# Kernel tuning notes

Measured on AMD Instinct MI355X. Metric: run time of the kernel, lower is better.

Reference implementation:

```python
import jax, jax.numpy as jnp
import numpy as np

N_NODES = 50000
N_PAIRS = 625000
F = 128

def setup_inputs() -> dict:
    key = jax.random.key(0)
    k1, k2, k3, k4, k5 = jax.random.split(key, 5)
    x = jax.random.normal(k1, (N_NODES, F), dtype=jnp.float32)
    alpha_ij = jax.random.normal(k2, (N_PAIRS,), dtype=jnp.float32)
    idx_i = jax.random.randint(k3, (N_PAIRS,), 0, N_NODES, dtype=jnp.int32)
    idx_j = jax.random.randint(k4, (N_PAIRS,), 0, N_NODES, dtype=jnp.int32)
    # Dense(F, use_bias=False) kernel, shape (F_in, F_out)
    W = jax.random.normal(k5, (F, F), dtype=jnp.float32) / np.sqrt(F)
    return {"x": x, "alpha_ij": alpha_ij, "idx_i": idx_i, "idx_j": idx_j, "W": W}

def reference(x, alpha_ij, idx_i, idx_j, W):
    # dense projection on nodes (n,F) @ (F,F) -> (n,F)
    v = jnp.matmul(x, W)
    # gather neighbor values, scale by attention coeff: (n_pairs, F)
    msg = alpha_ij[:, None] * v[idx_j]
    # scatter-sum back to center atoms
    return jax.ops.segment_sum(msg, segment_ids=idx_i, num_segments=x.shape[0])
```

## Files before the change

kernel.cpp:

```cpp
#include <hip/hip_runtime.h>
#include <stdint.h>

#define FDIM 128
#define BR 64
#define SLOTS 48
#define NB_C 196
#define QC 4096
#define PPB 2048
#define P2SPLIT 4

typedef short  s8v   __attribute__((ext_vector_type(8)));
typedef float  f4v   __attribute__((ext_vector_type(4)));
typedef unsigned short u8v __attribute__((ext_vector_type(8)));

__device__ __forceinline__ unsigned short f2bf(float f) {
    union { float f; uint32_t u; } c; c.f = f;
    uint32_t u = c.u;
    return (unsigned short)((u + 0x7fffu + ((u >> 16) & 1u)) >> 16);
}
__device__ __forceinline__ float bflo2f(uint32_t g) {
    union { uint32_t u; float f; } c; c.u = g << 16; return c.f;
}
__device__ __forceinline__ float bfhi2f(uint32_t g) {
    union { uint32_t u; float f; } c; c.u = g & 0xffff0000u; return c.f;
}

__global__ __launch_bounds__(256) void prep(const float* __restrict__ W,
                                            unsigned short* __restrict__ Wt,
                                            int* __restrict__ cnt,
                                            int* __restrict__ gcur,
                                            int n_nodes) {
    int i = blockIdx.x * 256 + threadIdx.x;
    if (i < FDIM * FDIM) {
        int n = i & 127, k = i >> 7;
        Wt[n * FDIM + k] = f2bf(W[k * FDIM + n]);
    }
    if (i < n_nodes) cnt[i] = 0;
    if (i < NB_C)    gcur[i] = 0;
}

__global__ __launch_bounds__(256) void fused_gemm_pass1(
        const float* __restrict__ x,
        const unsigned short* __restrict__ Wt,
        unsigned short* __restrict__ v,
        const int* __restrict__ idx_i,
        const int* __restrict__ idx_j,
        const float* __restrict__ alpha,
        int* __restrict__ gcur,
        unsigned long long* __restrict__ qrec,
        int n_rows, int n_pairs, int GB) {
    __shared__ unsigned short As[BR][FDIM + 8];

    if ((int)blockIdx.x >= GB) {
        __shared__ int hist[NB_C];
        __shared__ int base_s[NB_C];
        const int t = threadIdx.x;
        const int start = (blockIdx.x - GB) * PPB;

        if (t < NB_C) hist[t] = 0;
        __syncthreads();

        unsigned long long rec[8];
        int bkt[8];
#pragma unroll
        for (int i = 0; i < 8; ++i) {
            int p = start + t + i * 256;
            bkt[i] = -1;
            if (p < n_pairs) {
                int ii = idx_i[p];
                int b  = ii >> 8;
                bkt[i] = b;
                rec[i] = (unsigned long long)(uint32_t)(idx_j[p] | ((ii & 255) << 16) | (b << 24))
                       | ((unsigned long long)(uint32_t)__float_as_int(alpha[p]) << 32);
                atomicAdd(&hist[b], 1);
            }
        }
        __syncthreads();
        if (t < NB_C) {
            int h = hist[t];
            base_s[t] = (h > 0) ? atomicAdd(&gcur[t], h) : 0;
            hist[t] = 0;
        }
        __syncthreads();
#pragma unroll
        for (int i = 0; i < 8; ++i) {
            int b = bkt[i];
            if (b >= 0) {
                int lp  = atomicAdd(&hist[b], 1);
                int pos = base_s[b] + lp;
                if (pos < QC)
                    qrec[(size_t)b * QC + pos] = rec[i];
            }
        }
        return;
    }

    const int t = threadIdx.x;
    const int row0 = blockIdx.x * BR;
    {
        int r  = t >> 2;
        int c0 = (t & 3) * 32;
        int grow = row0 + r;
        const float* src = x + (size_t)grow * FDIM + c0;
#pragma unroll
        for (int it = 0; it < 4; ++it) {
            float4 xa = make_float4(0.f, 0.f, 0.f, 0.f);
            float4 xb = make_float4(0.f, 0.f, 0.f, 0.f);
            if (grow < n_rows) {
                xa = *(const float4*)(src + it * 8);
                xb = *(const float4*)(src + it * 8 + 4);
            }
            u8v pk;
            pk[0] = f2bf(xa.x); pk[1] = f2bf(xa.y); pk[2] = f2bf(xa.z); pk[3] = f2bf(xa.w);
            pk[4] = f2bf(xb.x); pk[5] = f2bf(xb.y); pk[6] = f2bf(xb.z); pk[7] = f2bf(xb.w);
            *(u8v*)(&As[r][c0 + it * 8]) = pk;
        }
    }
    __syncthreads();

    const int w    = t >> 6;
    const int lane = t & 63;
    const int rt   = (w & 1) * 32;
    const int ct   = (w >> 1) * 64;
    const int lrow = lane & 15;
    const int kq   = (lane >> 4) * 8;

    f4v acc[2][4];
#pragma unroll
    for (int i = 0; i < 2; ++i)
#pragma unroll
        for (int j = 0; j < 4; ++j)
            acc[i][j] = (f4v){0.f, 0.f, 0.f, 0.f};

#pragma unroll
    for (int ks = 0; ks < 4; ++ks) {
        const int k0 = ks * 32 + kq;
        const unsigned short* wb = Wt + (size_t)(ct + lrow) * FDIM + k0;
        s8v b0 = *(const s8v*)(wb);
        s8v b1 = *(const s8v*)(wb + 16 * FDIM);
        s8v b2 = *(const s8v*)(wb + 32 * FDIM);
        s8v b3 = *(const s8v*)(wb + 48 * FDIM);
        s8v a0 = *(const s8v*)(&As[rt + lrow][k0]);
        s8v a1 = *(const s8v*)(&As[rt + 16 + lrow][k0]);
        acc[0][0] = __builtin_amdgcn_mfma_f32_16x16x32_bf16(a0, b0, acc[0][0], 0, 0, 0);
        acc[0][1] = __builtin_amdgcn_mfma_f32_16x16x32_bf16(a0, b1, acc[0][1], 0, 0, 0);
        acc[0][2] = __builtin_amdgcn_mfma_f32_16x16x32_bf16(a0, b2, acc[0][2], 0, 0, 0);
        acc[0][3] = __builtin_amdgcn_mfma_f32_16x16x32_bf16(a0, b3, acc[0][3], 0, 0, 0);
        acc[1][0] = __builtin_amdgcn_mfma_f32_16x16x32_bf16(a1, b0, acc[1][0], 0, 0, 0);
        acc[1][1] = __builtin_amdgcn_mfma_f32_16x16x32_bf16(a1, b1, acc[1][1], 0, 0, 0);
        acc[1][2] = __builtin_amdgcn_mfma_f32_16x16x32_bf16(a1, b2, acc[1][2], 0, 0, 0);
        acc[1][3] = __builtin_amdgcn_mfma_f32_16x16x32_bf16(a1, b3, acc[1][3], 0, 0, 0);
    }

    const int quad = lane >> 4;
#pragma unroll
    for (int i = 0; i < 2; ++i) {
#pragma unroll
        for (int r = 0; r < 4; ++r) {
            int row = row0 + rt + i * 16 + quad * 4 + r;
            if (row < n_rows) {
#pragma unroll
                for (int j = 0; j < 4; ++j) {
                    int col = ct + j * 16 + lrow;
                    v[(size_t)row * FDIM + col] = f2bf(acc[i][j][r]);
                }
            }
        }
    }
}

__global__ __launch_bounds__(256) void pass2(const unsigned long long* __restrict__ qrec,
                                             const int* __restrict__ gcur,
                                             int* __restrict__ cnt,
                                             int2* __restrict__ pairs) {
    const int c    = blockIdx.x / P2SPLIT;
    const int part = blockIdx.x % P2SPLIT;
    int nrec = gcur[c];
    nrec = (nrec > QC) ? QC : nrec;
    const int lo = (nrec * part) / P2SPLIT;
    const int hi = (nrec * (part + 1)) / P2SPLIT;
    const unsigned long long* q = qrec + (size_t)c * QC;

    for (int k = lo + threadIdx.x; k < hi; k += 256) {
        unsigned long long r = q[k];
        uint32_t lowb = (uint32_t)r;
        int j    = lowb & 0xffff;
        int node = c * 256 + ((lowb >> 16) & 0xff);
        int pos  = atomicAdd(&cnt[node], 1);
        if (pos < SLOTS) {
            int2 pr;
            pr.x = j;
            pr.y = (int)(r >> 32);
            pairs[(size_t)node * SLOTS + pos] = pr;
        }
    }
}

__global__ __launch_bounds__(256) void aggregate(const unsigned short* __restrict__ v,
                                                 const int* __restrict__ cnt,
                                                 const int2* __restrict__ pairs,
                                                 float* __restrict__ out,
                                                 int n_nodes) {
    const int node = blockIdx.x * 4 + (threadIdx.x >> 6);
    const int lane = threadIdx.x & 63;
    if (node >= n_nodes) return;

    int deg = cnt[node];
    deg = (deg > SLOTS) ? SLOTS : deg;
    const int2* pp = pairs + (size_t)node * SLOTS;

    float ax = 0.f, ay = 0.f;
    int k = 0;
    for (; k + 4 <= deg; k += 4) {
        int4 q0 = *(const int4*)(pp + k);
        int4 q1 = *(const int4*)(pp + k + 2);
        float a0 = __int_as_float(q0.y);
        float a1 = __int_as_float(q0.w);
        float a2 = __int_as_float(q1.y);
        float a3 = __int_as_float(q1.w);
        uint32_t g0 = *(const uint32_t*)(v + (size_t)q0.x * FDIM + lane * 2);
        uint32_t g1 = *(const uint32_t*)(v + (size_t)q0.z * FDIM + lane * 2);
        uint32_t g2 = *(const uint32_t*)(v + (size_t)q1.x * FDIM + lane * 2);
        uint32_t g3 = *(const uint32_t*)(v + (size_t)q1.z * FDIM + lane * 2);
        ax += a0 * bflo2f(g0) + a1 * bflo2f(g1);
        ay += a0 * bfhi2f(g0) + a1 * bfhi2f(g1);
        ax += a2 * bflo2f(g2) + a3 * bflo2f(g3);
        ay += a2 * bfhi2f(g2) + a3 * bfhi2f(g3);
    }
    if (k + 2 <= deg) {
        int4 q0 = *(const int4*)(pp + k);
        float a0 = __int_as_float(q0.y);
        float a1 = __int_as_float(q0.w);
        uint32_t g0 = *(const uint32_t*)(v + (size_t)q0.x * FDIM + lane * 2);
        uint32_t g1 = *(const uint32_t*)(v + (size_t)q0.z * FDIM + lane * 2);
        ax += a0 * bflo2f(g0) + a1 * bflo2f(g1);
        ay += a0 * bfhi2f(g0) + a1 * bfhi2f(g1);
        k += 2;
    }
    if (k < deg) {
        int2 p0 = pp[k];
        float a0 = __int_as_float(p0.y);
        uint32_t g0 = *(const uint32_t*)(v + (size_t)p0.x * FDIM + lane * 2);
        ax += a0 * bflo2f(g0);
        ay += a0 * bfhi2f(g0);
    }
    float2 r;
    r.x = ax;
    r.y = ay;
    *(float2*)(out + (size_t)node * FDIM + lane * 2) = r;
}

extern "C" void kernel_launch(void* const* d_in, const int* in_sizes, int n_in,
                              void* d_out, int out_size, void* d_ws, size_t ws_size,
                              hipStream_t stream) {
    const float* x     = (const float*)d_in[0];
    const float* alpha = (const float*)d_in[1];
    const int*   idx_i = (const int*)d_in[2];
    const int*   idx_j = (const int*)d_in[3];
    const float* W     = (const float*)d_in[4];

    const int n_nodes = in_sizes[0] / FDIM;
    const int n_pairs = in_sizes[1];

    char* ws = (char*)d_ws;
    size_t off = 0;
    auto carve = [&](size_t bytes) {
        char* p = ws + off;
        off += (bytes + 255) & ~(size_t)255;
        return p;
    };
    unsigned short* v  = (unsigned short*)carve((size_t)n_nodes * FDIM * sizeof(unsigned short));
    unsigned short* Wt = (unsigned short*)carve((size_t)FDIM * FDIM * sizeof(unsigned short));
    int*  cnt  = (int*)carve((size_t)n_nodes * sizeof(int));
    int*  gcur = (int*)carve((size_t)NB_C * sizeof(int));
    unsigned long long* qrec =
        (unsigned long long*)carve((size_t)NB_C * QC * sizeof(unsigned long long));
    int2* pairs = (int2*)carve((size_t)n_nodes * SLOTS * sizeof(int2));
    float* out  = (float*)d_out;

    int pb = (max(n_nodes, FDIM * FDIM) + 255) / 256;
    prep<<<pb, 256, 0, stream>>>(W, Wt, cnt, gcur, n_nodes);

    int GB = (n_nodes + BR - 1) / BR;
    int PB = (n_pairs + PPB - 1) / PPB;
    fused_gemm_pass1<<<GB + PB, 256, 0, stream>>>(x, Wt, v, idx_i, idx_j, alpha,
                                                  gcur, qrec, n_nodes, n_pairs, GB);

    pass2<<<NB_C * P2SPLIT, 256, 0, stream>>>(qrec, gcur, cnt, pairs);

    int ablocks = (n_nodes + 3) / 4;
    aggregate<<<ablocks, 256, 0, stream>>>(v, cnt, pairs, out, n_nodes);
}
```

Before: 151.7 us.

## Replace global bucket queues with per-block sorted runs and prefix offsets

```diff
diff --git a/kernel.cpp b/kernel.cpp
--- a/kernel.cpp
+++ b/kernel.cpp
@@ -5,9 +5,8 @@
 #define BR 64
 #define SLOTS 48
 #define NB_C 196
-#define QC 4096
 #define PPB 2048
-#define P2SPLIT 4
+#define SROW 200
 
 typedef short  s8v   __attribute__((ext_vector_type(8)));
 typedef float  f4v   __attribute__((ext_vector_type(4)));
@@ -28,7 +27,6 @@
 __global__ __launch_bounds__(256) void prep(const float* __restrict__ W,
                                             unsigned short* __restrict__ Wt,
                                             int* __restrict__ cnt,
-                                            int* __restrict__ gcur,
                                             int n_nodes) {
     int i = blockIdx.x * 256 + threadIdx.x;
     if (i < FDIM * FDIM) {
@@ -36,7 +34,6 @@
         Wt[n * FDIM + k] = f2bf(W[k * FDIM + n]);
     }
     if (i < n_nodes) cnt[i] = 0;
-    if (i < NB_C)    gcur[i] = 0;
 }
 
 __global__ __launch_bounds__(256) void fused_gemm_pass1(
@@ -46,16 +43,18 @@
         const int* __restrict__ idx_i,
         const int* __restrict__ idx_j,
         const float* __restrict__ alpha,
-        int* __restrict__ gcur,
-        unsigned long long* __restrict__ qrec,
+        unsigned long long* __restrict__ qrec2,
+        int* __restrict__ starts_g,
         int n_rows, int n_pairs, int GB) {
     __shared__ unsigned short As[BR][FDIM + 8];
 
     if ((int)blockIdx.x >= GB) {
         __shared__ int hist[NB_C];
-        __shared__ int base_s[NB_C];
-        const int t = threadIdx.x;
-        const int start = (blockIdx.x - GB) * PPB;
+        __shared__ int s[256];
+        __shared__ unsigned long long srec[PPB];
+        const int t  = threadIdx.x;
+        const int bb = blockIdx.x - GB;
+        const int start = bb * PPB;
 
         if (t < NB_C) hist[t] = 0;
         __syncthreads();
@@ -70,28 +69,41 @@
                 int ii = idx_i[p];
                 int b  = ii >> 8;
                 bkt[i] = b;
-                rec[i] = (unsigned long long)(uint32_t)(idx_j[p] | ((ii & 255) << 16) | (b << 24))
+                rec[i] = (unsigned long long)(uint32_t)(idx_j[p] | ((ii & 255) << 16))
                        | ((unsigned long long)(uint32_t)__float_as_int(alpha[p]) << 32);
                 atomicAdd(&hist[b], 1);
             }
         }
         __syncthreads();
-        if (t < NB_C) {
-            int h = hist[t];
-            base_s[t] = (h > 0) ? atomicAdd(&gcur[t], h) : 0;
-            hist[t] = 0;
-        }
-        __syncthreads();
+
+        int hv = (t < NB_C) ? hist[t] : 0;
+        s[t] = hv;
+        __syncthreads();
+#pragma unroll
+        for (int d = 1; d < 256; d <<= 1) {
+            int tmp = (t >= d) ? s[t - d] : 0;
+            __syncthreads();
+            s[t] += tmp;
+            __syncthreads();
+        }
+        const int excl = s[t] - hv;
+        if (t <= NB_C) starts_g[bb * SROW + t] = excl;
+        if (t < NB_C)  hist[t] = excl;
+        const int valid = s[255];
+        __syncthreads();
+
 #pragma unroll
         for (int i = 0; i < 8; ++i) {
-            int b = bkt[i];
-            if (b >= 0) {
-                int lp  = atomicAdd(&hist[b], 1);
-                int pos = base_s[b] + lp;
-                if (pos < QC)
-                    qrec[(size_t)b * QC + pos] = rec[i];
-            }
-        }
+            if (bkt[i] >= 0) {
+                int pos = atomicAdd(&hist[bkt[i]], 1);
+                srec[pos] = rec[i];
+            }
+        }
+        __syncthreads();
+
+        unsigned long long* dst = qrec2 + (size_t)bb * PPB;
+        for (int k = t; k < valid; k += 256)
+            dst[k] = srec[k];
         return;
     }
 
@@ -169,29 +181,30 @@
     }
 }
 
-__global__ __launch_bounds__(256) void pass2(const unsigned long long* __restrict__ qrec,
-                                             const int* __restrict__ gcur,
+__global__ __launch_bounds__(256) void pass2(const unsigned long long* __restrict__ qrec2,
+                                             const int* __restrict__ starts_g,
                                              int* __restrict__ cnt,
-                                             int2* __restrict__ pairs) {
-    const int c    = blockIdx.x / P2SPLIT;
-    const int part = blockIdx.x % P2SPLIT;
-    int nrec = gcur[c];
-    nrec = (nrec > QC) ? QC : nrec;
-    const int lo = (nrec * part) / P2SPLIT;
-    const int hi = (nrec * (part + 1)) / P2SPLIT;
-    const unsigned long long* q = qrec + (size_t)c * QC;
-
-    for (int k = lo + threadIdx.x; k < hi; k += 256) {
-        unsigned long long r = q[k];
-        uint32_t lowb = (uint32_t)r;
-        int j    = lowb & 0xffff;
-        int node = c * 256 + ((lowb >> 16) & 0xff);
-        int pos  = atomicAdd(&cnt[node], 1);
-        if (pos < SLOTS) {
-            int2 pr;
-            pr.x = j;
-            pr.y = (int)(r >> 32);
-            pairs[(size_t)node * SLOTS + pos] = pr;
+                                             int2* __restrict__ pairs,
+                                             int nblk) {
+    const int c    = blockIdx.x >> 1;
+    const int part = blockIdx.x & 1;
+    const int t    = threadIdx.x;
+
+    for (int bb = part + 2 * t; bb < nblk; bb += 512) {
+        int s0 = starts_g[bb * SROW + c];
+        int s1 = starts_g[bb * SROW + c + 1];
+        const unsigned long long* q = qrec2 + (size_t)bb * PPB;
+        for (int k = s0; k < s1; ++k) {
+            unsigned long long r = q[k];
+            uint32_t lo = (uint32_t)r;
+            int node = (c << 8) + ((lo >> 16) & 0xff);
+            int pos  = atomicAdd(&cnt[node], 1);
+            if (pos < SLOTS) {
+                int2 pr;
+                pr.x = lo & 0xffff;
+                pr.y = (int)(r >> 32);
+                pairs[(size_t)node * SLOTS + pos] = pr;
+            }
         }
     }
 }
@@ -261,6 +274,7 @@
 
     const int n_nodes = in_sizes[0] / FDIM;
     const int n_pairs = in_sizes[1];
+    const int PB      = (n_pairs + PPB - 1) / PPB;
 
     char* ws = (char*)d_ws;
     size_t off = 0;
@@ -271,22 +285,21 @@
     };
     unsigned short* v  = (unsigned short*)carve((size_t)n_nodes * FDIM * sizeof(unsigned short));
     unsigned short* Wt = (unsigned short*)carve((size_t)FDIM * FDIM * sizeof(unsigned short));
-    int*  cnt  = (int*)carve((size_t)n_nodes * sizeof(int));
-    int*  gcur = (int*)carve((size_t)NB_C * sizeof(int));
-    unsigned long long* qrec =
-        (unsigned long long*)carve((size_t)NB_C * QC * sizeof(unsigned long long));
+    int*  cnt = (int*)carve((size_t)n_nodes * sizeof(int));
+    unsigned long long* qrec2 =
+        (unsigned long long*)carve((size_t)PB * PPB * sizeof(unsigned long long));
+    int*  starts_g = (int*)carve((size_t)PB * SROW * sizeof(int));
     int2* pairs = (int2*)carve((size_t)n_nodes * SLOTS * sizeof(int2));
     float* out  = (float*)d_out;
 
     int pb = (max(n_nodes, FDIM * FDIM) + 255) / 256;
-    prep<<<pb, 256, 0, stream>>>(W, Wt, cnt, gcur, n_nodes);
+    prep<<<pb, 256, 0, stream>>>(W, Wt, cnt, n_nodes);
 
     int GB = (n_nodes + BR - 1) / BR;
-    int PB = (n_pairs + PPB - 1) / PPB;
     fused_gemm_pass1<<<GB + PB, 256, 0, stream>>>(x, Wt, v, idx_i, idx_j, alpha,
-                                                  gcur, qrec, n_nodes, n_pairs, GB);
-
-    pass2<<<NB_C * P2SPLIT, 256, 0, stream>>>(qrec, gcur, cnt, pairs);
+                                                  qrec2, starts_g, n_nodes, n_pairs, GB);
+
+    pass2<<<NB_C * 2, 256, 0, stream>>>(qrec2, starts_g, cnt, pairs, PB);
 
     int ablocks = (n_nodes + 3) / 4;
     aggregate<<<ablocks, 256, 0, stream>>>(v, cnt, pairs, out, n_nodes);
```

New measurement: 155.9 us. +2.8%, slower.
